# Kernel optimization log

Measured on AMD Instinct MI355X. Metric: run time of the kernel, lower is better.

The kernel has to match this reference:

```python
import jax, jax.numpy as jnp
import numpy as np

NUM_HEADS = 16
D_MODEL = 1024
DEPTH = D_MODEL // NUM_HEADS
THRESHOLD = 0.1
BATCH = 2
SEQ = 2048


def setup_inputs() -> dict:
    key = jax.random.key(0)
    ks = jax.random.split(key, 9)
    w_scale = 1.0 / np.sqrt(D_MODEL)
    Q = jax.random.normal(ks[0], (BATCH, SEQ, D_MODEL), dtype=jnp.float32)
    T = jax.random.normal(ks[1], (BATCH, SEQ, D_MODEL), dtype=jnp.float32)
    V = jax.random.normal(ks[2], (BATCH, SEQ, D_MODEL), dtype=jnp.float32)
    Wq = jax.random.normal(ks[3], (NUM_HEADS, D_MODEL, DEPTH), dtype=jnp.float32) * w_scale
    Wk = jax.random.normal(ks[4], (NUM_HEADS, D_MODEL, DEPTH), dtype=jnp.float32) * w_scale
    Wv = jax.random.normal(ks[5], (NUM_HEADS, D_MODEL, DEPTH), dtype=jnp.float32) * w_scale
    Wo = jax.random.normal(ks[6], (D_MODEL, D_MODEL), dtype=jnp.float32) * w_scale
    bq = jnp.zeros((NUM_HEADS, DEPTH), dtype=jnp.float32)
    bk = jnp.zeros((NUM_HEADS, DEPTH), dtype=jnp.float32)
    bv = jnp.zeros((NUM_HEADS, DEPTH), dtype=jnp.float32)
    bo = jnp.zeros((D_MODEL,), dtype=jnp.float32)
    return {"Q": Q, "T": T, "V": V, "Wq": Wq, "bq": bq, "Wk": Wk, "bk": bk,
            "Wv": Wv, "bv": bv, "Wo": Wo, "bo": bo}


def reference(Q, T, V, Wq, bq, Wk, bk, Wv, bv, Wo, bo):
    # Per-head projections (stacked over heads): [B,S,D] x [H,D,E] -> [B,H,S,E]
    q = jnp.einsum('bsd,hde->bhse', Q, Wq) + bq[None, :, None, :]
    k = jnp.einsum('bsd,hde->bhse', T, Wk) + bk[None, :, None, :]
    v = jnp.einsum('bsd,hde->bhse', V, Wv) + bv[None, :, None, :]

    # Raw scores (NOT pre-scaled): [B,H,S,S]
    scores = jnp.einsum('bhqe,bhke->bhqk', q, k)
    # tf.where(A>thr, A, -2**32 * cast(A>thr)) -> failing entries become 0
    scores = jnp.where(scores > THRESHOLD, scores, jnp.zeros((), scores.dtype))
    # M = 1 - lower_band(ones): +1 on strictly upper-triangular entries
    seq = scores.shape[-1]
    upper = jnp.triu(jnp.ones((seq, seq), dtype=scores.dtype), k=1)
    scores = (scores + upper) / jnp.sqrt(jnp.asarray(DEPTH, scores.dtype))

    attn = jax.nn.softmax(scores, axis=-1)
    out = jnp.einsum('bhqk,bhke->bhqe', attn, v)  # [B,H,S,E]
    B, H, S, E = out.shape
    concat = out.transpose(0, 2, 1, 3).reshape(B, S, H * E)  # [B,S,D]
    return concat @ Wo + bo
```

## Files before the change

### kernel.cpp

```cpp
#include <hip/hip_runtime.h>
#include <stdint.h>


typedef __attribute__((ext_vector_type(8))) short bf16x8;
typedef __attribute__((ext_vector_type(4))) float f32x4;

#define DEVFN static __device__ __forceinline__

static constexpr int S_ = 2048;
static constexpr int H_ = 16;

DEVFN unsigned short f2bf(float x) {
  union { float f; uint32_t u; } v; v.f = x;
  const uint32_t r = v.u + 0x7fffu + ((v.u >> 16) & 1u);
  return (unsigned short)(r >> 16);
}

DEVFN f32x4 fzero() { f32x4 v = {0.f, 0.f, 0.f, 0.f}; return v; }

DEVFN void gld_lds16(const void* g, void* lds) {
  __builtin_amdgcn_global_load_lds(
      (const __attribute__((address_space(1))) void*)g,
      (__attribute__((address_space(3))) void*)lds, 16, 0, 0);
}

__global__ void prep_weights(const float* __restrict__ Wq, const float* __restrict__ Wk,
                             const float* __restrict__ Wv, const float* __restrict__ Wo,
                             unsigned short* __restrict__ dstBase) {
  const int z = blockIdx.z;
  const float* src = (z == 0) ? Wq : (z == 1) ? Wk : (z == 2) ? Wv : Wo;
  unsigned short* dst = dstBase + (size_t)z * (1024u * 1024u);
  const int idx = blockIdx.x * 256 + threadIdx.x;
  const int c = idx & 1023;
  const int d0 = (idx >> 10) << 3;
  unsigned short hv[8];
#pragma unroll
  for (int t = 0; t < 8; ++t) {
    const int d = d0 + t;
    const float v = (z < 3) ? src[(size_t)((c >> 6) * 1024 + d) * 64 + (c & 63)]
                            : src[(size_t)d * 1024 + c];
    hv[t] = f2bf(v);
  }
  *(uint4*)(dst + (size_t)c * 1024 + d0) = *(const uint4*)hv;
}

__global__ __launch_bounds__(256, 3)
void proj_gemm(const float* __restrict__ Qm, const float* __restrict__ Tm,
               const float* __restrict__ Vm, const unsigned short* __restrict__ Wt,
               const float* __restrict__ bq, const float* __restrict__ bk,
               const float* __restrict__ bv, unsigned short* __restrict__ qb,
               unsigned short* __restrict__ kb, unsigned short* __restrict__ vtb) {
  __shared__ unsigned short At[2][128 * 32];
  __shared__ unsigned short Bt[2][128 * 32];

  const int tid = threadIdx.x;
  const int lane = tid & 63;
  const int w = tid >> 6;
  const int g = lane >> 4, c = lane & 15;
  const int wm = w >> 1, wn = w & 1;

  const int m0 = blockIdx.x * 128;
  const int proj = blockIdx.y >> 3;
  const int n0 = (blockIdx.y & 7) * 128;

  const float* Asrc = (proj == 0) ? Qm : (proj == 1) ? Tm : Vm;
  const unsigned short* W = Wt + (size_t)proj * (1024u * 1024u);

  f32x4 acc[4][4];
#pragma unroll
  for (int i = 0; i < 4; ++i)
#pragma unroll
    for (int j = 0; j < 4; ++j) acc[i][j] = fzero();

  const int ar = tid >> 1;
  const int ah = tid & 1;
  const int swzA = (ar >> 1) & 3;
  const float* aBase = Asrc + (size_t)(m0 + ar) * 1024 + ah * 16;
  const int brow0 = w * 32 + (lane >> 2);
  const int bch = lane & 3;

  auto stage = [&](int kt, int buf) {
#pragma unroll
    for (int u = 0; u < 2; ++u) {
      const int row = brow0 + u * 16;
      const int ch = bch ^ ((row >> 1) & 3);
      gld_lds16(W + (size_t)(n0 + row) * 1024 + kt * 32 + ch * 8,
                &Bt[buf][(w * 32 + u * 16) * 32]);
    }
    const float* s = aBase + kt * 32;
    const float4 f0 = ((const float4*)s)[0];
    const float4 f1 = ((const float4*)s)[1];
    const float4 f2 = ((const float4*)s)[2];
    const float4 f3 = ((const float4*)s)[3];
    uint32_t d0, d1, d2, d3, d4, d5, d6, d7;
    asm("v_cvt_pk_bf16_f32 %0, %1, %2" : "=v"(d0) : "v"(f0.x), "v"(f0.y));
    asm("v_cvt_pk_bf16_f32 %0, %1, %2" : "=v"(d1) : "v"(f0.z), "v"(f0.w));
    asm("v_cvt_pk_bf16_f32 %0, %1, %2" : "=v"(d2) : "v"(f1.x), "v"(f1.y));
    asm("v_cvt_pk_bf16_f32 %0, %1, %2" : "=v"(d3) : "v"(f1.z), "v"(f1.w));
    asm("v_cvt_pk_bf16_f32 %0, %1, %2" : "=v"(d4) : "v"(f2.x), "v"(f2.y));
    asm("v_cvt_pk_bf16_f32 %0, %1, %2" : "=v"(d5) : "v"(f2.z), "v"(f2.w));
    asm("v_cvt_pk_bf16_f32 %0, %1, %2" : "=v"(d6) : "v"(f3.x), "v"(f3.y));
    asm("v_cvt_pk_bf16_f32 %0, %1, %2" : "=v"(d7) : "v"(f3.z), "v"(f3.w));
    uint4 lo; lo.x = d0; lo.y = d1; lo.z = d2; lo.w = d3;
    uint4 hi; hi.x = d4; hi.y = d5; hi.z = d6; hi.w = d7;
    *(uint4*)&At[buf][ar * 32 + ((ah * 2 + 0) ^ swzA) * 8] = lo;
    *(uint4*)&At[buf][ar * 32 + ((ah * 2 + 1) ^ swzA) * 8] = hi;
  };

  stage(0, 0);
  __syncthreads();

  for (int kt = 0; kt < 32; ++kt) {
    const int buf = kt & 1;
    if (kt < 31) stage(kt + 1, buf ^ 1);

    bf16x8 af[4], bfr[4];
#pragma unroll
    for (int mi = 0; mi < 4; ++mi) {
      const int row = wm * 64 + mi * 16 + c;
      af[mi] = *(const bf16x8*)&At[buf][row * 32 + ((g ^ ((row >> 1) & 3))) * 8];
    }
#pragma unroll
    for (int ni = 0; ni < 4; ++ni) {
      const int row = wn * 64 + ni * 16 + c;
      bfr[ni] = *(const bf16x8*)&Bt[buf][row * 32 + ((g ^ ((row >> 1) & 3))) * 8];
    }
#pragma unroll
    for (int mi = 0; mi < 4; ++mi)
#pragma unroll
      for (int ni = 0; ni < 4; ++ni)
        acc[mi][ni] = __builtin_amdgcn_mfma_f32_16x16x32_bf16(af[mi], bfr[ni],
                                                              acc[mi][ni], 0, 0, 0);
    __syncthreads();
  }

  const float* bias = (proj == 0) ? bq : (proj == 1) ? bk : bv;
#pragma unroll
  for (int ni = 0; ni < 4; ++ni) {
    const int colb = n0 + wn * 64 + ni * 16 + c;
    const float bc = bias[colb];
    const int hh = colb >> 6, e = colb & 63;
#pragma unroll
    for (int mi = 0; mi < 4; ++mi) {
#pragma unroll
      for (int r = 0; r < 4; ++r) {
        const int row = m0 + wm * 64 + mi * 16 + g * 4 + r;
        const int bb = row >> 11, s = row & 2047;
        const float val = acc[mi][ni][r] + bc;
        if (proj < 2) {
          unsigned short* d = (proj == 0) ? qb : kb;
          d[(((size_t)(bb * H_ + hh)) * S_ + s) * 64 + e] = f2bf(val);
        } else {
          vtb[(((size_t)(bb * H_ + hh)) * 64 + e) * S_ + s] = f2bf(val);
        }
      }
    }
  }
}

__global__ __launch_bounds__(256, 4)
void attn_kernel(const unsigned short* __restrict__ qb,
                 const unsigned short* __restrict__ kb,
                 const unsigned short* __restrict__ vtb,
                 unsigned short* __restrict__ att) {
  __shared__ unsigned short Kt[2][64 * 64];
  __shared__ unsigned short Vt[2][64 * 64];
  __shared__ unsigned short Pt[4][16 * 64];

  const int tid = threadIdx.x;
  const int lane = tid & 63;
  const int w = tid >> 6;
  const int g = lane >> 4, c = lane & 15;

  const int orig = blockIdx.x;
  const int logical = ((orig & 7) << 7) | (orig >> 3);
  const int qblk = logical & 31;
  const int bh = logical >> 5;
  const int hh = bh & 15, bz = bh >> 4;

  const int q0w = qblk * 64 + w * 16;
  const unsigned short* qh = qb + (size_t)bh * S_ * 64;
  const unsigned short* kh = kb + (size_t)bh * S_ * 64;
  const unsigned short* vh = vtb + (size_t)bh * 64 * S_;

  bf16x8 aq[2];
#pragma unroll
  for (int t = 0; t < 2; ++t)
    aq[t] = *(const bf16x8*)&qh[(size_t)(q0w + c) * 64 + t * 32 + g * 8];

  f32x4 O[4];
#pragma unroll
  for (int ne = 0; ne < 4; ++ne) O[ne] = fzero();
  float l_lane = 0.f;

  constexpr float L2E = 1.4426950408889634f;
  const float S2 = 0.125f * L2E;
  const float B2 = 0.125f * L2E;
  const int iq = q0w + c;

  const int srow = w * 8 + (lane >> 3);
  const int sch = lane & 7;

  {
#pragma unroll
    for (int u = 0; u < 2; ++u) {
      const int row = u * 32 + srow;
      gld_lds16(kh + (size_t)row * 64 + (sch ^ (row & 7)) * 8,
                &Kt[0][(u * 32 + w * 8) * 64]);
      gld_lds16(vh + (size_t)row * S_ + (sch ^ (row & 7)) * 8,
                &Vt[0][(u * 32 + w * 8) * 64]);
    }
  }
  __syncthreads();

  for (int jt = 0; jt < 32; ++jt) {
    const int cur = jt & 1;
    const int j0 = jt * 64;

    if (jt < 31) {
      const int jn = j0 + 64;
#pragma unroll
      for (int u = 0; u < 2; ++u) {
        const int row = u * 32 + srow;
        gld_lds16(kh + (size_t)(jn + row) * 64 + (sch ^ (row & 7)) * 8,
                  &Kt[cur ^ 1][(u * 32 + w * 8) * 64]);
        gld_lds16(vh + (size_t)row * S_ + jn + (sch ^ (row & 7)) * 8,
                  &Vt[cur ^ 1][(u * 32 + w * 8) * 64]);
      }
    }

    f32x4 sa[4];
#pragma unroll
    for (int mi = 0; mi < 4; ++mi) sa[mi] = fzero();
    __builtin_amdgcn_s_setprio(1);
#pragma unroll
    for (int ks = 0; ks < 2; ++ks) {
#pragma unroll
      for (int mi = 0; mi < 4; ++mi) {
        const int row = mi * 16 + c;
        const bf16x8 ka =
            *(const bf16x8*)&Kt[cur][row * 64 + ((ks * 4 + g) ^ (row & 7)) * 8];
        sa[mi] = __builtin_amdgcn_mfma_f32_16x16x32_bf16(ka, aq[ks], sa[mi], 0, 0, 0);
      }
    }
    __builtin_amdgcn_s_setprio(0);

    float pe[16];
    const bool allUp = (j0 >= q0w + 16);
    const bool noneUp = (j0 + 63 <= q0w);
    if (allUp || noneUp) {
      const float bb = allUp ? B2 : 0.f;
#pragma unroll
      for (int i = 0; i < 16; ++i) {
        const float v = sa[i >> 2][i & 3];
        const float arg = (v > 0.1f) ? __builtin_fmaf(v, S2, bb) : bb;
        pe[i] = __builtin_amdgcn_exp2f(arg);
      }
    } else {
#pragma unroll
      for (int mi = 0; mi < 4; ++mi)
#pragma unroll
        for (int r = 0; r < 4; ++r) {
          const float v = sa[mi][r];
          const float bb = (j0 + mi * 16 + g * 4 + r > iq) ? B2 : 0.f;
          const float arg = (v > 0.1f) ? __builtin_fmaf(v, S2, bb) : bb;
          pe[mi * 4 + r] = __builtin_amdgcn_exp2f(arg);
        }
    }

    {
      float s01 = pe[0] + pe[1], s23 = pe[2] + pe[3];
      float s45 = pe[4] + pe[5], s67 = pe[6] + pe[7];
      float s89 = pe[8] + pe[9], sab = pe[10] + pe[11];
      float scd = pe[12] + pe[13], sef = pe[14] + pe[15];
      l_lane += ((s01 + s23) + (s45 + s67)) + ((s89 + sab) + (scd + sef));
    }

#pragma unroll
    for (int mi = 0; mi < 4; ++mi) {
      uint2 d;
      asm("v_cvt_pk_bf16_f32 %0, %1, %2"
          : "=v"(d.x) : "v"(pe[mi * 4 + 0]), "v"(pe[mi * 4 + 1]));
      asm("v_cvt_pk_bf16_f32 %0, %1, %2"
          : "=v"(d.y) : "v"(pe[mi * 4 + 2]), "v"(pe[mi * 4 + 3]));
      const int pc = (2 * mi + (g >> 1)) ^ (c & 7);
      *(uint2*)&Pt[w][c * 64 + pc * 8 + (g & 1) * 4] = d;
    }
    asm volatile("s_waitcnt lgkmcnt(0)" ::: "memory");
    __builtin_amdgcn_sched_barrier(0);

    __builtin_amdgcn_s_setprio(1);
#pragma unroll
    for (int ks = 0; ks < 2; ++ks) {
      const bf16x8 pa =
          *(const bf16x8*)&Pt[w][c * 64 + (((ks * 4 + g) ^ (c & 7))) * 8];
#pragma unroll
      for (int ne = 0; ne < 4; ++ne) {
        const int e = ne * 16 + c;
        const bf16x8 bv8 =
            *(const bf16x8*)&Vt[cur][e * 64 + ((ks * 4 + g) ^ (e & 7)) * 8];
        O[ne] = __builtin_amdgcn_mfma_f32_16x16x32_bf16(pa, bv8, O[ne], 0, 0, 0);
      }
    }
    __builtin_amdgcn_s_setprio(0);
    __syncthreads();
  }

  float l = l_lane;
  l += __shfl_xor(l, 16);
  l += __shfl_xor(l, 32);
  const float invl = 1.f / l;
  const int base = (lane >> 2) & 12;
  float il[4];
#pragma unroll
  for (int r = 0; r < 4; ++r) il[r] = __shfl(invl, base + r);
#pragma unroll
  for (int r = 0; r < 4; ++r) {
    const int qg = q0w + g * 4 + r;
    const size_t ro = ((size_t)(bz * S_ + qg)) * 1024 + hh * 64;
#pragma unroll
    for (int ne = 0; ne < 4; ++ne)
      att[ro + ne * 16 + c] = f2bf(O[ne][r] * il[r]);
  }
}

__global__ __launch_bounds__(256, 3)
void out_gemm(const unsigned short* __restrict__ att,
              const unsigned short* __restrict__ WoT,
              const float* __restrict__ bo, float* __restrict__ outp) {
  __shared__ unsigned short At[2][128 * 32];
  __shared__ unsigned short Bt[2][128 * 32];

  const int tid = threadIdx.x;
  const int lane = tid & 63;
  const int w = tid >> 6;
  const int g = lane >> 4, c = lane & 15;
  const int wm = w >> 1, wn = w & 1;
  const int m0 = blockIdx.x * 128;
  const int n0 = blockIdx.y * 128;

  f32x4 acc[4][4];
#pragma unroll
  for (int i = 0; i < 4; ++i)
#pragma unroll
    for (int j = 0; j < 4; ++j) acc[i][j] = fzero();

  const int brow0 = w * 32 + (lane >> 2);
  const int bch = lane & 3;

  auto stage = [&](int kt, int buf) {
#pragma unroll
    for (int u = 0; u < 2; ++u) {
      const int row = brow0 + u * 16;
      const int ch = bch ^ ((row >> 1) & 3);
      gld_lds16(att + (size_t)(m0 + row) * 1024 + kt * 32 + ch * 8,
                &At[buf][(w * 32 + u * 16) * 32]);
      gld_lds16(WoT + (size_t)(n0 + row) * 1024 + kt * 32 + ch * 8,
                &Bt[buf][(w * 32 + u * 16) * 32]);
    }
  };

  stage(0, 0);
  __syncthreads();

  for (int kt = 0; kt < 32; ++kt) {
    const int buf = kt & 1;
    if (kt < 31) stage(kt + 1, buf ^ 1);

    bf16x8 af[4], bfr[4];
#pragma unroll
    for (int mi = 0; mi < 4; ++mi) {
      const int row = wm * 64 + mi * 16 + c;
      af[mi] = *(const bf16x8*)&At[buf][row * 32 + ((g ^ ((row >> 1) & 3))) * 8];
    }
#pragma unroll
    for (int ni = 0; ni < 4; ++ni) {
      const int row = wn * 64 + ni * 16 + c;
      bfr[ni] = *(const bf16x8*)&Bt[buf][row * 32 + ((g ^ ((row >> 1) & 3))) * 8];
    }
#pragma unroll
    for (int mi = 0; mi < 4; ++mi)
#pragma unroll
      for (int ni = 0; ni < 4; ++ni)
        acc[mi][ni] = __builtin_amdgcn_mfma_f32_16x16x32_bf16(af[mi], bfr[ni],
                                                              acc[mi][ni], 0, 0, 0);
    __syncthreads();
  }

#pragma unroll
  for (int ni = 0; ni < 4; ++ni) {
    const int colb = n0 + wn * 64 + ni * 16 + c;
    const float bc = bo[colb];
#pragma unroll
    for (int mi = 0; mi < 4; ++mi)
#pragma unroll
      for (int r = 0; r < 4; ++r) {
        const int row = m0 + wm * 64 + mi * 16 + g * 4 + r;
        outp[(size_t)row * 1024 + colb] = acc[mi][ni][r] + bc;
      }
  }
}

extern "C" void kernel_launch(void* const* d_in, const int* in_sizes, int n_in,
                              void* d_out, int out_size, void* d_ws, size_t ws_size,
                              hipStream_t stream) {
  const float* Q  = (const float*)d_in[0];
  const float* T  = (const float*)d_in[1];
  const float* V  = (const float*)d_in[2];
  const float* Wq = (const float*)d_in[3];
  const float* bq = (const float*)d_in[4];
  const float* Wk = (const float*)d_in[5];
  const float* bk = (const float*)d_in[6];
  const float* Wv = (const float*)d_in[7];
  const float* bv = (const float*)d_in[8];
  const float* Wo = (const float*)d_in[9];
  const float* bo = (const float*)d_in[10];

  const size_t MB = 1024ull * 1024ull;
  if (ws_size < 40 * MB) return;

  uint8_t* ws = (uint8_t*)d_ws;
  unsigned short* Wt  = (unsigned short*)(ws);
  unsigned short* qb  = (unsigned short*)(ws + 8 * MB);
  unsigned short* kb  = (unsigned short*)(ws + 16 * MB);
  unsigned short* vtb = (unsigned short*)(ws + 24 * MB);
  unsigned short* attb = (unsigned short*)(ws + 32 * MB);

  prep_weights<<<dim3(512, 1, 4), 256, 0, stream>>>(Wq, Wk, Wv, Wo, Wt);
  proj_gemm<<<dim3(32, 24), 256, 0, stream>>>(Q, T, V, Wt, bq, bk, bv, qb, kb, vtb);
  attn_kernel<<<dim3(1024), 256, 0, stream>>>(qb, kb, vtb, attb);
  out_gemm<<<dim3(32, 8), 256, 0, stream>>>(attb, Wt + 3ull * 1024ull * 1024ull,
                                            bo, (float*)d_out);
}
```

Measured before the change: 145.6 us.

## Pre-convert Q/T/V activations to bf16 and stage via direct global-to-LDS loads

Adds a separate conversion kernel that turns the fp32 Q, T, V inputs into bf16 buffers, reusing the output and attention scratch space as temporary storage. The projection GEMM then loads A tiles with global_load_lds the same way it loads weights, instead of doing fp32 loads, register conversion and LDS stores inside the main loop. Launch bounds rise to 4 blocks per SM, and the staging row mapping is changed in both GEMMs. The cost is an extra kernel launch plus a full extra read and write pass over the activations.

```diff
diff --git a/kernel.cpp b/kernel.cpp
--- a/kernel.cpp
+++ b/kernel.cpp
@@ -44,9 +44,29 @@
   *(uint4*)(dst + (size_t)c * 1024 + d0) = *(const uint4*)hv;
 }
 
-__global__ __launch_bounds__(256, 3)
-void proj_gemm(const float* __restrict__ Qm, const float* __restrict__ Tm,
-               const float* __restrict__ Vm, const unsigned short* __restrict__ Wt,
+__global__ void convert_a(const float* __restrict__ Qm, const float* __restrict__ Tm,
+                          const float* __restrict__ Vm, unsigned short* __restrict__ aq,
+                          unsigned short* __restrict__ at2, unsigned short* __restrict__ av) {
+  const int z = blockIdx.z;
+  const float* s = (z == 0) ? Qm : (z == 1) ? Tm : Vm;
+  unsigned short* d = (z == 0) ? aq : (z == 1) ? at2 : av;
+  const size_t i = ((size_t)blockIdx.x * 256 + threadIdx.x) * 8;
+  const float4 f0 = *(const float4*)(s + i);
+  const float4 f1 = *(const float4*)(s + i + 4);
+  uint32_t d0, d1, d2, d3;
+  asm("v_cvt_pk_bf16_f32 %0, %1, %2" : "=v"(d0) : "v"(f0.x), "v"(f0.y));
+  asm("v_cvt_pk_bf16_f32 %0, %1, %2" : "=v"(d1) : "v"(f0.z), "v"(f0.w));
+  asm("v_cvt_pk_bf16_f32 %0, %1, %2" : "=v"(d2) : "v"(f1.x), "v"(f1.y));
+  asm("v_cvt_pk_bf16_f32 %0, %1, %2" : "=v"(d3) : "v"(f1.z), "v"(f1.w));
+  uint4 o; o.x = d0; o.y = d1; o.z = d2; o.w = d3;
+  *(uint4*)(d + i) = o;
+}
+
+__global__ __launch_bounds__(256, 4)
+void proj_gemm(const unsigned short* __restrict__ Aq,
+               const unsigned short* __restrict__ At2,
+               const unsigned short* __restrict__ Av,
+               const unsigned short* __restrict__ Wt,
                const float* __restrict__ bq, const float* __restrict__ bk,
                const float* __restrict__ bv, unsigned short* __restrict__ qb,
                unsigned short* __restrict__ kb, unsigned short* __restrict__ vtb) {
@@ -63,7 +83,7 @@
   const int proj = blockIdx.y >> 3;
   const int n0 = (blockIdx.y & 7) * 128;
 
-  const float* Asrc = (proj == 0) ? Qm : (proj == 1) ? Tm : Vm;
+  const unsigned short* Abf = (proj == 0) ? Aq : (proj == 1) ? At2 : Av;
   const unsigned short* W = Wt + (size_t)proj * (1024u * 1024u);
 
   f32x4 acc[4][4];
@@ -72,39 +92,19 @@
 #pragma unroll
     for (int j = 0; j < 4; ++j) acc[i][j] = fzero();
 
-  const int ar = tid >> 1;
-  const int ah = tid & 1;
-  const int swzA = (ar >> 1) & 3;
-  const float* aBase = Asrc + (size_t)(m0 + ar) * 1024 + ah * 16;
-  const int brow0 = w * 32 + (lane >> 2);
-  const int bch = lane & 3;
+  const int srow = lane >> 2;
+  const int sch = lane & 3;
 
   auto stage = [&](int kt, int buf) {
 #pragma unroll
     for (int u = 0; u < 2; ++u) {
-      const int row = brow0 + u * 16;
-      const int ch = bch ^ ((row >> 1) & 3);
+      const int row = u * 64 + w * 16 + srow;
+      const int ch = sch ^ ((row >> 1) & 3);
+      gld_lds16(Abf + (size_t)(m0 + row) * 1024 + kt * 32 + ch * 8,
+                &At[buf][(u * 64 + w * 16) * 32]);
       gld_lds16(W + (size_t)(n0 + row) * 1024 + kt * 32 + ch * 8,
-                &Bt[buf][(w * 32 + u * 16) * 32]);
-    }
-    const float* s = aBase + kt * 32;
-    const float4 f0 = ((const float4*)s)[0];
-    const float4 f1 = ((const float4*)s)[1];
-    const float4 f2 = ((const float4*)s)[2];
-    const float4 f3 = ((const float4*)s)[3];
-    uint32_t d0, d1, d2, d3, d4, d5, d6, d7;
-    asm("v_cvt_pk_bf16_f32 %0, %1, %2" : "=v"(d0) : "v"(f0.x), "v"(f0.y));
-    asm("v_cvt_pk_bf16_f32 %0, %1, %2" : "=v"(d1) : "v"(f0.z), "v"(f0.w));
-    asm("v_cvt_pk_bf16_f32 %0, %1, %2" : "=v"(d2) : "v"(f1.x), "v"(f1.y));
-    asm("v_cvt_pk_bf16_f32 %0, %1, %2" : "=v"(d3) : "v"(f1.z), "v"(f1.w));
-    asm("v_cvt_pk_bf16_f32 %0, %1, %2" : "=v"(d4) : "v"(f2.x), "v"(f2.y));
-    asm("v_cvt_pk_bf16_f32 %0, %1, %2" : "=v"(d5) : "v"(f2.z), "v"(f2.w));
-    asm("v_cvt_pk_bf16_f32 %0, %1, %2" : "=v"(d6) : "v"(f3.x), "v"(f3.y));
-    asm("v_cvt_pk_bf16_f32 %0, %1, %2" : "=v"(d7) : "v"(f3.z), "v"(f3.w));
-    uint4 lo; lo.x = d0; lo.y = d1; lo.z = d2; lo.w = d3;
-    uint4 hi; hi.x = d4; hi.y = d5; hi.z = d6; hi.w = d7;
-    *(uint4*)&At[buf][ar * 32 + ((ah * 2 + 0) ^ swzA) * 8] = lo;
-    *(uint4*)&At[buf][ar * 32 + ((ah * 2 + 1) ^ swzA) * 8] = hi;
+                &Bt[buf][(u * 64 + w * 16) * 32]);
+    }
   };
 
   stage(0, 0);
@@ -345,18 +345,18 @@
 #pragma unroll
     for (int j = 0; j < 4; ++j) acc[i][j] = fzero();
 
-  const int brow0 = w * 32 + (lane >> 2);
-  const int bch = lane & 3;
+  const int srow = lane >> 2;
+  const int sch = lane & 3;
 
   auto stage = [&](int kt, int buf) {
 #pragma unroll
     for (int u = 0; u < 2; ++u) {
-      const int row = brow0 + u * 16;
-      const int ch = bch ^ ((row >> 1) & 3);
+      const int row = u * 64 + w * 16 + srow;
+      const int ch = sch ^ ((row >> 1) & 3);
       gld_lds16(att + (size_t)(m0 + row) * 1024 + kt * 32 + ch * 8,
-                &At[buf][(w * 32 + u * 16) * 32]);
+                &At[buf][(u * 64 + w * 16) * 32]);
       gld_lds16(WoT + (size_t)(n0 + row) * 1024 + kt * 32 + ch * 8,
-                &Bt[buf][(w * 32 + u * 16) * 32]);
+                &Bt[buf][(u * 64 + w * 16) * 32]);
     }
   };
 
@@ -426,8 +426,14 @@
   unsigned short* vtb = (unsigned short*)(ws + 24 * MB);
   unsigned short* attb = (unsigned short*)(ws + 32 * MB);
 
+  unsigned short* aQ = (unsigned short*)d_out;
+  unsigned short* aT = aQ + 4ull * 1024ull * 1024ull;
+  unsigned short* aV = attb;
+
   prep_weights<<<dim3(512, 1, 4), 256, 0, stream>>>(Wq, Wk, Wv, Wo, Wt);
-  proj_gemm<<<dim3(32, 24), 256, 0, stream>>>(Q, T, V, Wt, bq, bk, bv, qb, kb, vtb);
+  convert_a<<<dim3(2048, 1, 3), 256, 0, stream>>>(Q, T, V, aQ, aT, aV);
+  proj_gemm<<<dim3(32, 24), 256, 0, stream>>>(aQ, aT, aV, Wt, bq, bk, bv,
+                                              qb, kb, vtb);
   attn_kernel<<<dim3(1024), 256, 0, stream>>>(qb, kb, vtb, attb);
   out_gemm<<<dim3(32, 8), 256, 0, stream>>>(attb, Wt + 3ull * 1024ull * 1024ull,
                                             bo, (float*)d_out);
```

After: 146.4 us. No clear change (+0.5%).
